# Performance work log

Measured on AMD Instinct MI355X. Metric: run time of the kernel, lower is better.

## Reference

```python
import jax, jax.numpy as jnp
import numpy as np

EPS = 1e-5
RES = [12000, 9000, 6000, 4000]
CH = [9, 64, 128, 256]
SKIPS = 3
FC_N = 128


def batchnorm(x, g, b):
    # train-mode BatchNorm2d over (batch, face) dims; x: [B, C, F]
    m = x.mean(axis=(0, 2), keepdims=True)
    v = x.var(axis=(0, 2), keepdims=True)
    xn = (x - m) * jax.lax.rsqrt(v + EPS)
    return xn * g[None, :, None] + b[None, :, None]


def mesh_conv(x, nbr, w):
    # x: [B, C, F]; nbr: [F, 3] neighbor face ids; w: [O, C, 4]
    n = x[:, :, nbr]                      # [B, C, F, 3] irregular gather
    n1, n2, n3 = n[..., 0], n[..., 1], n[..., 2]
    G = jnp.stack([
        x,
        n1 + n2 + n3,
        jnp.abs(n1 - n2) + jnp.abs(n2 - n3) + jnp.abs(n3 - n1),
        jnp.maximum(jnp.maximum(n1, n2), n3),
    ], axis=-1)                           # [B, C, F, 4] symmetric features
    return jnp.einsum('ocj,bcfj->bof', w, G)


def mres_conv(x, nbr, wc, ws, bng, bnb):
    # MResConvFace: conv0 -> skips x (bn(relu) -> conv) -> +skip -> relu
    x = mesh_conv(x, nbr, wc)
    x1 = x
    for i in range(SKIPS):
        x = batchnorm(jax.nn.relu(x), bng[i], bnb[i])
        x = mesh_conv(x, nbr, ws[i])
    return jax.nn.relu(x + x1)


def setup_inputs() -> dict:
    key = jax.random.key(0)
    ks = jax.random.split(key, 64)
    it = iter(range(64))
    d = {}
    d['x'] = jax.random.normal(ks[next(it)], (8, CH[0], RES[0]), dtype=jnp.float32)
    for i in range(3):
        d[f'nbr{i}'] = jax.random.randint(ks[next(it)], (RES[i], 3), 0, RES[i], dtype=jnp.int32)
        d[f'pool{i}'] = jax.random.randint(ks[next(it)], (RES[i + 1], 3), 0, RES[i], dtype=jnp.int32)
    for i in range(3):
        cin, cout = CH[i], CH[i + 1]
        d[f'wc{i}'] = jax.random.normal(ks[next(it)], (cout, cin, 4), dtype=jnp.float32) * (1.0 / np.sqrt(4 * cin))
        d[f'ws{i}'] = jax.random.normal(ks[next(it)], (SKIPS, cout, cout, 4), dtype=jnp.float32) * (1.0 / np.sqrt(4 * cout))
        d[f'bng{i}'] = jnp.ones((SKIPS, cout), dtype=jnp.float32)
        d[f'bnb{i}'] = jnp.zeros((SKIPS, cout), dtype=jnp.float32)
        d[f'ng{i}'] = jnp.ones((cout,), dtype=jnp.float32)
        d[f'nb{i}'] = jnp.zeros((cout,), dtype=jnp.float32)
    d['fc1_w'] = jax.random.normal(ks[next(it)], (FC_N, CH[-1]), dtype=jnp.float32) * (1.0 / np.sqrt(CH[-1]))
    d['fc1_b'] = jnp.zeros((FC_N,), dtype=jnp.float32)
    d['fc2_w'] = jax.random.normal(ks[next(it)], (1, FC_N), dtype=jnp.float32) * (1.0 / np.sqrt(FC_N))
    d['fc2_b'] = jnp.zeros((1,), dtype=jnp.float32)
    return d


def reference(x, nbr0, nbr1, nbr2, pool0, pool1, pool2,
              wc0, ws0, bng0, bnb0, ng0, nb0,
              wc1, ws1, bng1, bnb1, ng1, nb1,
              wc2, ws2, bng2, bnb2, ng2, nb2,
              fc1_w, fc1_b, fc2_w, fc2_b):
    nbrs = [nbr0, nbr1, nbr2]
    pools = [pool0, pool1, pool2]
    wcs, wss = [wc0, wc1, wc2], [ws0, ws1, ws2]
    bngs, bnbs = [bng0, bng1, bng2], [bnb0, bnb1, bnb2]
    ngs, nbs = [ng0, ng1, ng2], [nb0, nb1, nb2]
    for i in range(3):
        x = mres_conv(x, nbrs[i], wcs[i], wss[i], bngs[i], bnbs[i])
        x = jax.nn.relu(batchnorm(x, ngs[i], nbs[i]))
        x = x[:, :, pools[i]].mean(axis=-1)   # MeshPoolFace: collapse 3 faces -> 1
    x = x.mean(axis=-1)                        # global AvgPool1d over faces -> [B, C]
    h = jax.nn.relu(x @ fc1_w.T + fc1_b)
    return jax.nn.sigmoid(h @ fc2_w.T + fc2_b)  # [B, 1]
```

## Files before the change

kernel.cpp:

```cpp
#include <hip/hip_runtime.h>
#include <math.h>

#define NPART 64
#define TILE_F 16

typedef unsigned short u16;
typedef __attribute__((ext_vector_type(8))) short short8;
typedef __attribute__((ext_vector_type(4))) float f32x4;

__device__ __forceinline__ float relu_(float v){ return fmaxf(v, 0.f); }

__device__ __forceinline__ u16 f2bf(float x){
  unsigned u = __float_as_uint(x);
  u = (u + 0x7fffu + ((u >> 16) & 1u)) >> 16;
  return (u16)u;
}

static __device__ __forceinline__ f32x4 mfma_bf16(short8 a, short8 b, f32x4 c){
  asm("v_mfma_f32_16x16x32_bf16 %0, %1, %2, %0" : "+v"(c) : "v"(a), "v"(b));
  return c;
}

template<int CIN,int COUT,int WR,int NWR,bool BN,bool STATS,bool RES>
__global__ __launch_bounds__(NWR*(COUT/64)*64) void mconv_kernel(
    const float* __restrict__ xin, const int* __restrict__ nbr,
    const u16* __restrict__ wbf,
    const float* __restrict__ ps_in, const float* __restrict__ gamma,
    const float* __restrict__ beta, const float* __restrict__ res,
    float* __restrict__ out, float* __restrict__ psum,
    int F, float invN)
{
  constexpr int nWc = COUT/64;
  constexpr int T   = NWR*nWc*64;
  constexpr int BR  = NWR*WR;
  constexpr int K   = 4*CIN;
  constexpr int NSTEP = CIN/16;
  constexpr int ITEMS = (BR*4)/T;
  constexpr int NRF   = WR/16;

  __shared__ __align__(16) u16 Gs[2][BR*64];
  __shared__ float ls[STATS?COUT:1], lq[STATS?COUT:1];
  __shared__ float aS[BN?CIN:1], dS[BN?CIN:1];

  const int t=threadIdx.x, lane=t&63, wid=t>>6;
  const int wm=wid/nWc, wc=wid%nWc;
  const int l15=lane&15, kq=lane>>4;

  const int batch = blockIdx.x & 7;
  const int row0  = (blockIdx.x >> 3) * BR;

  if (BN){
    for (int c=t;c<CIN;c+=T){
      float s=0.f,q=0.f;
      #pragma unroll 4
      for (int p=0;p<NPART;p++){ s+=ps_in[p*256+c]; q+=ps_in[(NPART+p)*256+c]; }
      float m=s*invN, v=q*invN-m*m;
      float ai=gamma[c]*rsqrtf(v+1e-5f);
      aS[c]=ai; dS[c]=beta[c]-m*ai;
    }
  }
  if (STATS){ for (int i=t;i<COUT;i+=T){ ls[i]=0.f; lq[i]=0.f; } }
  __syncthreads();

  const float *P0[ITEMS],*P1[ITEMS],*P2[ITEMS],*P3[ITEMS];
  #pragma unroll
  for (int i=0;i<ITEMS;i++){
    int idx=i*T+t, gr=idx>>2, c4q=idx&3;
    int f=row0+gr;
    if (f>=F) f=F-1;
    int i1=nbr[f*3+0], i2=nbr[f*3+1], i3=nbr[f*3+2];
    const float* xb=xin+(size_t)batch*F*CIN+c4q*4;
    P0[i]=xb+(size_t)f *CIN; P1[i]=xb+(size_t)i1*CIN;
    P2[i]=xb+(size_t)i2*CIN; P3[i]=xb+(size_t)i3*CIN;
  }

  const u16* wp = wbf + (size_t)(wc*64+l15)*K + kq*8;
  auto BLD=[&](int cg,int j)->short8{
    return *(const short8*)(wp + (size_t)cg*16*K + (size_t)j*32);
  };
  auto ADS=[&](int pb,int rr,int h)->short8{
    int r=wm*WR+rr*16+l15;
    int sl=h*4+kq;
    return *(const short8*)&Gs[pb][(size_t)r*64 + (size_t)((sl^(r&7))*8)];
  };
  auto GLD=[&](int s,float4 (&g)[ITEMS][4]){
    #pragma unroll
    for (int i=0;i<ITEMS;i++){
      g[i][0]=*(const float4*)(P0[i]+s*16);
      g[i][1]=*(const float4*)(P1[i]+s*16);
      g[i][2]=*(const float4*)(P2[i]+s*16);
      g[i][3]=*(const float4*)(P3[i]+s*16);
    }
  };
  auto BLDW=[&](int pb,int s,float4 (&g)[ITEMS][4]){
    #pragma unroll
    for (int i=0;i<ITEMS;i++){
      int idx=i*T+t, gr=idx>>2, c4q=idx&3;
      float4 S=g[i][0],N1=g[i][1],N2=g[i][2],N3=g[i][3];
      if (BN){
        float4 a4=*(const float4*)&aS[s*16+c4q*4];
        float4 d4=*(const float4*)&dS[s*16+c4q*4];
        S.x =fmaf(relu_(S.x ),a4.x,d4.x); S.y =fmaf(relu_(S.y ),a4.y,d4.y);
        S.z =fmaf(relu_(S.z ),a4.z,d4.z); S.w =fmaf(relu_(S.w ),a4.w,d4.w);
        N1.x=fmaf(relu_(N1.x),a4.x,d4.x); N1.y=fmaf(relu_(N1.y),a4.y,d4.y);
        N1.z=fmaf(relu_(N1.z),a4.z,d4.z); N1.w=fmaf(relu_(N1.w),a4.w,d4.w);
        N2.x=fmaf(relu_(N2.x),a4.x,d4.x); N2.y=fmaf(relu_(N2.y),a4.y,d4.y);
        N2.z=fmaf(relu_(N2.z),a4.z,d4.z); N2.w=fmaf(relu_(N2.w),a4.w,d4.w);
        N3.x=fmaf(relu_(N3.x),a4.x,d4.x); N3.y=fmaf(relu_(N3.y),a4.y,d4.y);
        N3.z=fmaf(relu_(N3.z),a4.z,d4.z); N3.w=fmaf(relu_(N3.w),a4.w,d4.w);
      }
      short8 lo,hi;
      #define FEAT(dst,i0,sv,av,bv,cv) \
        dst[i0+0]=(short)f2bf(sv); \
        dst[i0+1]=(short)f2bf(av+bv+cv); \
        dst[i0+2]=(short)f2bf(fabsf(av-bv)+fabsf(bv-cv)+fabsf(cv-av)); \
        dst[i0+3]=(short)f2bf(fmaxf(fmaxf(av,bv),cv));
      FEAT(lo,0,S.x,N1.x,N2.x,N3.x)
      FEAT(lo,4,S.y,N1.y,N2.y,N3.y)
      FEAT(hi,0,S.z,N1.z,N2.z,N3.z)
      FEAT(hi,4,S.w,N1.w,N2.w,N3.w)
      #undef FEAT
      u16* rowp=&Gs[pb][(size_t)gr*64];
      *(short8*)&rowp[(size_t)(((2*c4q  )^(gr&7))*8)]=lo;
      *(short8*)&rowp[(size_t)(((2*c4q+1)^(gr&7))*8)]=hi;
    }
  };

  f32x4 acc[NRF][4];
  #pragma unroll
  for (int rr=0;rr<NRF;rr++)
    #pragma unroll
    for (int cg=0;cg<4;cg++){ f32x4 z={0.f,0.f,0.f,0.f}; acc[rr][cg]=z; }

  short8 B0[4],B1[4];
  #pragma unroll
  for (int cg=0;cg<4;cg++) B0[cg]=BLD(cg,0);
  #pragma unroll
  for (int cg=0;cg<4;cg++) B1[cg]=BLD(cg,1);

  { float4 g0[ITEMS][4]; GLD(0,g0); BLDW(0,0,g0); }
  __syncthreads();

  #pragma unroll 2
  for (int s=0;s<NSTEP;s++){
    const int pb=s&1;
    float4 g[ITEMS][4];
    if (s+1<NSTEP) GLD(s+1,g);
    short8 A[NRF];
    #pragma unroll
    for (int rr=0;rr<NRF;rr++) A[rr]=ADS(pb,rr,0);
    #pragma unroll
    for (int rr=0;rr<NRF;rr++)
      #pragma unroll
      for (int cg=0;cg<4;cg++) acc[rr][cg]=mfma_bf16(A[rr],B0[cg],acc[rr][cg]);
    if (s+1<NSTEP){
      #pragma unroll
      for (int cg=0;cg<4;cg++) B0[cg]=BLD(cg,2*(s+1));
    }
    #pragma unroll
    for (int rr=0;rr<NRF;rr++) A[rr]=ADS(pb,rr,1);
    #pragma unroll
    for (int rr=0;rr<NRF;rr++)
      #pragma unroll
      for (int cg=0;cg<4;cg++) acc[rr][cg]=mfma_bf16(A[rr],B1[cg],acc[rr][cg]);
    if (s+1<NSTEP){
      #pragma unroll
      for (int cg=0;cg<4;cg++) B1[cg]=BLD(cg,2*(s+1)+1);
      BLDW(pb^1,s+1,g);
    }
    __syncthreads();
  }

  const size_t bbase=(size_t)batch*F;
  #pragma unroll
  for (int cg=0;cg<4;cg++){
    const int col=wc*64+cg*16+l15;
    float rs=0.f,rq=0.f;
    #pragma unroll
    for (int rr=0;rr<NRF;rr++){
      const int r0=row0 + wm*WR + rr*16 + kq*4;
      #pragma unroll
      for (int q=0;q<4;q++){
        int r=r0+q;
        if (r<F){
          size_t idx=(bbase+r)*COUT+col;
          float v=acc[rr][cg][q];
          if (RES){ v += res[idx]; v = relu_(v); }
          out[idx]=v;
          if (STATS){ float rv = RES ? v : relu_(v); rs+=rv; rq+=rv*rv; }
        }
      }
    }
    if (STATS){ atomicAdd(&ls[col],rs); atomicAdd(&lq[col],rq); }
  }
  if (STATS){
    __syncthreads();
    const int part=blockIdx.x&(NPART-1);
    for (int i=t;i<COUT;i+=T){
      atomicAdd(&psum[(size_t)part*256+i],ls[i]);
      atomicAdd(&psum[(size_t)(NPART+part)*256+i],lq[i]);
    }
  }
}

template<int CIN,int COUT,bool BN,bool STATS>
__global__ __launch_bounds__(256) void conv_kernel(
    const float* __restrict__ xin, const int* __restrict__ nbr,
    const float* __restrict__ Wt, const float* __restrict__ bn_a,
    const float* __restrict__ bn_d,
    float* __restrict__ out, float* __restrict__ psum, int F)
{
  constexpr int K = 4*CIN;
  constexpr int ROWLEN = K + 4;
  __shared__ float Gs[TILE_F][ROWLEN];
  __shared__ int   nI[TILE_F*3];
  __shared__ float ls[STATS?COUT:1];
  __shared__ float lq[STATS?COUT:1];
  const int t = threadIdx.x;
  const int fbase = blockIdx.x*TILE_F;
  const int b = blockIdx.y;
  const float* __restrict__ xb = xin + (size_t)b*F*CIN;

  if (t < TILE_F*3){ int fi=t/3, j=t-fi*3; int fg=fbase+fi; nI[t]=(fg<F)?nbr[fg*3+j]:0; }
  if (STATS){ for (int i=t;i<COUT;i+=256){ ls[i]=0.f; lq[i]=0.f; } }
  __syncthreads();

  for (int idx=t; idx<TILE_F*CIN; idx+=256){
    int fi=idx/CIN, c=idx-fi*CIN;
    int fg=fbase+fi;
    float* dst=&Gs[fi][4*c];
    if (fg<F){
      int i1=nI[fi*3], i2=nI[fi*3+1], i3=nI[fi*3+2];
      float s =xb[(size_t)fg*CIN+c];
      float v1=xb[(size_t)i1*CIN+c];
      float v2=xb[(size_t)i2*CIN+c];
      float v3=xb[(size_t)i3*CIN+c];
      if (BN){ float a=bn_a[c], dd=bn_d[c];
        s=fmaf(relu_(s),a,dd); v1=fmaf(relu_(v1),a,dd);
        v2=fmaf(relu_(v2),a,dd); v3=fmaf(relu_(v3),a,dd); }
      dst[0]=s; dst[1]=v1+v2+v3;
      dst[2]=fabsf(v1-v2)+fabsf(v2-v3)+fabsf(v3-v1);
      dst[3]=fmaxf(fmaxf(v1,v2),v3);
    } else { dst[0]=0.f;dst[1]=0.f;dst[2]=0.f;dst[3]=0.f; }
  }
  __syncthreads();

  constexpr int OQ=COUT/4;
  constexpr int R=256/OQ;
  constexpr int FPT=TILE_F/R;
  const int col=t%OQ, row=t/OQ;
  const int o0=col*4, f0=row*FPT;
  float4 acc[FPT];
  #pragma unroll
  for (int fi=0;fi<FPT;fi++){ acc[fi].x=0.f;acc[fi].y=0.f;acc[fi].z=0.f;acc[fi].w=0.f; }

  for (int k=0;k<K;k+=4){
    float4 w0=*(const float4*)&Wt[(size_t)(k+0)*COUT+o0];
    float4 w1=*(const float4*)&Wt[(size_t)(k+1)*COUT+o0];
    float4 w2=*(const float4*)&Wt[(size_t)(k+2)*COUT+o0];
    float4 w3=*(const float4*)&Wt[(size_t)(k+3)*COUT+o0];
    #pragma unroll
    for (int fi=0;fi<FPT;fi++){
      float4 g=*(const float4*)&Gs[f0+fi][k];
      acc[fi].x=fmaf(g.x,w0.x,fmaf(g.y,w1.x,fmaf(g.z,w2.x,fmaf(g.w,w3.x,acc[fi].x))));
      acc[fi].y=fmaf(g.x,w0.y,fmaf(g.y,w1.y,fmaf(g.z,w2.y,fmaf(g.w,w3.y,acc[fi].y))));
      acc[fi].z=fmaf(g.x,w0.z,fmaf(g.y,w1.z,fmaf(g.z,w2.z,fmaf(g.w,w3.z,acc[fi].z))));
      acc[fi].w=fmaf(g.x,w0.w,fmaf(g.y,w1.w,fmaf(g.z,w2.w,fmaf(g.w,w3.w,acc[fi].w))));
    }
  }

  float4 rs={0,0,0,0}, rq={0,0,0,0};
  #pragma unroll
  for (int fi=0;fi<FPT;fi++){
    int fg=fbase+f0+fi;
    if (fg<F){
      *(float4*)&out[((size_t)b*F+fg)*COUT+o0]=acc[fi];
      if (STATS){
        float rx=relu_(acc[fi].x), ry=relu_(acc[fi].y);
        float rz=relu_(acc[fi].z), rw=relu_(acc[fi].w);
        rs.x+=rx; rs.y+=ry; rs.z+=rz; rs.w+=rw;
        rq.x+=rx*rx; rq.y+=ry*ry; rq.z+=rz*rz; rq.w+=rw*rw;
      }
    }
  }
  if (STATS){
    atomicAdd(&ls[o0+0],rs.x); atomicAdd(&ls[o0+1],rs.y);
    atomicAdd(&ls[o0+2],rs.z); atomicAdd(&ls[o0+3],rs.w);
    atomicAdd(&lq[o0+0],rq.x); atomicAdd(&lq[o0+1],rq.y);
    atomicAdd(&lq[o0+2],rq.z); atomicAdd(&lq[o0+3],rq.w);
    __syncthreads();
    int part=(blockIdx.y*gridDim.x+blockIdx.x)&(NPART-1);
    for (int i=t;i<COUT;i+=256){
      atomicAdd(&psum[(size_t)part*256+i], ls[i]);
      atomicAdd(&psum[(size_t)(NPART+part)*256+i], lq[i]);
    }
  }
}

__global__ __launch_bounds__(256) void pool_kernel(
    const float* __restrict__ z, const int* __restrict__ pl,
    const float* __restrict__ ps_in, const float* __restrict__ gamma,
    const float* __restrict__ beta,
    float* __restrict__ out, int C4, int F, int Fn, int n4, float invN)
{
  __shared__ float aS[256], dS[256];
  const int C=C4*4;
  const int t=threadIdx.x;
  if (t<C){
    float s=0.f,q=0.f;
    #pragma unroll 4
    for (int p=0;p<NPART;p++){ s+=ps_in[p*256+t]; q+=ps_in[(NPART+p)*256+t]; }
    float m=s*invN, v=q*invN-m*m;
    float ai=gamma[t]*rsqrtf(v+1e-5f);
    aS[t]=ai; dS[t]=beta[t]-m*ai;
  }
  __syncthreads();
  for (int i=blockIdx.x*256+t; i<n4; i+=gridDim.x*256){
    int c4=i%C4; int rest=i/C4; int p=rest%Fn; int b=rest/Fn;
    int p0=pl[p*3], p1=pl[p*3+1], p2=pl[p*3+2];
    float4 a4=*(const float4*)&aS[4*c4], d4=*(const float4*)&dS[4*c4];
    float4 v0=*(const float4*)&z[((size_t)b*F+p0)*C+4*c4];
    float4 v1=*(const float4*)&z[((size_t)b*F+p1)*C+4*c4];
    float4 v2=*(const float4*)&z[((size_t)b*F+p2)*C+4*c4];
    float4 r;
    r.x=(relu_(fmaf(v0.x,a4.x,d4.x))+relu_(fmaf(v1.x,a4.x,d4.x))+relu_(fmaf(v2.x,a4.x,d4.x)))*(1.f/3.f);
    r.y=(relu_(fmaf(v0.y,a4.y,d4.y))+relu_(fmaf(v1.y,a4.y,d4.y))+relu_(fmaf(v2.y,a4.y,d4.y)))*(1.f/3.f);
    r.z=(relu_(fmaf(v0.z,a4.z,d4.z))+relu_(fmaf(v1.z,a4.z,d4.z))+relu_(fmaf(v2.z,a4.z,d4.z)))*(1.f/3.f);
    r.w=(relu_(fmaf(v0.w,a4.w,d4.w))+relu_(fmaf(v1.w,a4.w,d4.w))+relu_(fmaf(v2.w,a4.w,d4.w)))*(1.f/3.f);
    *(float4*)&out[((size_t)b*Fn+p)*C+4*c4]=r;
  }
}

__global__ __launch_bounds__(256) void colsum_kernel(
    const float* __restrict__ x, float* __restrict__ bc, int F, int chunk)
{
  int b=blockIdx.y; int f0=blockIdx.x*chunk;
  int c=threadIdx.x;
  int fe=f0+chunk; if (fe>F) fe=F;
  float s=0.f;
  for (int f=f0;f<fe;f++) s+=x[((size_t)b*F+f)*256+c];
  atomicAdd(&bc[b*256+c], s);
}

__global__ __launch_bounds__(256) void head_kernel(
    const float* __restrict__ bc, const float* __restrict__ w1,
    const float* __restrict__ b1, const float* __restrict__ w2,
    const float* __restrict__ b2, float* __restrict__ outp, float invF)
{
  __shared__ float xm[8*256];
  __shared__ float h[8*128];
  int t=threadIdx.x;
  for (int i=t;i<2048;i+=256) xm[i]=bc[i]*invF;
  __syncthreads();
  #pragma unroll
  for (int r=0;r<4;r++){
    int idx=t+r*256; int b=idx>>7, j=idx&127;
    float s=b1[j];
    for (int c=0;c<256;c++) s=fmaf(xm[b*256+c],w1[j*256+c],s);
    h[idx]=relu_(s);
  }
  __syncthreads();
  if (t<8){
    float s=b2[0];
    for (int j=0;j<128;j++) s=fmaf(h[t*128+j],w2[j],s);
    outp[t]=1.f/(1.f+expf(-s));
  }
}

__global__ __launch_bounds__(256) void transpose_in_kernel(
    const float* __restrict__ x, float* __restrict__ xt, int F)
{
  int i=blockIdx.x*256+threadIdx.x;
  int total=8*9*F;
  if (i<total){ int f=i%F; int c=(i/F)%9; int b=i/(9*F);
    xt[((size_t)b*F+f)*9+c]=x[i]; }
}

__global__ __launch_bounds__(256) void transpose_w_kernel(
    const float* __restrict__ w, float* __restrict__ wt, int K, int COUT)
{
  int i=blockIdx.x*256+threadIdx.x;
  if (i<K*COUT){ int o=i/K, k=i-o*K; wt[(size_t)k*COUT+o]=w[i]; }
}

__global__ __launch_bounds__(256) void cvt_bf16_kernel(
    const float* __restrict__ w, u16* __restrict__ o, int n)
{
  int i=blockIdx.x*256+threadIdx.x;
  if (i<n) o[i]=f2bf(w[i]);
}


template<int CIN,int COUT,int WR,int NWR,bool BN,bool STATS,bool RES>
static void launch_mconv(const float* xin, const int* nbr, const u16* wbf,
                         const float* ps_in, const float* gamma, const float* beta,
                         const float* res, float* out, float* ps_out,
                         int F, float invN, hipStream_t stream)
{
  constexpr int T  = NWR*(COUT/64)*64;
  constexpr int BR = NWR*WR;
  int nb = (F + BR - 1)/BR;
  mconv_kernel<CIN,COUT,WR,NWR,BN,STATS,RES><<<8*nb, T, 0, stream>>>(
      xin,nbr,wbf,ps_in,gamma,beta,res,out,ps_out,F,invN);
}

extern "C" void kernel_launch(void* const* d_in, const int* in_sizes, int n_in,
                              void* d_out, int out_size, void* d_ws, size_t ws_size,
                              hipStream_t stream)
{
  const float* x    =(const float*)d_in[0];
  const int*  nbr0  =(const int*)d_in[1];
  const int*  pool0 =(const int*)d_in[2];
  const int*  nbr1  =(const int*)d_in[3];
  const int*  pool1 =(const int*)d_in[4];
  const int*  nbr2  =(const int*)d_in[5];
  const int*  pool2 =(const int*)d_in[6];
  const float* wc0  =(const float*)d_in[7];
  const float* ws0  =(const float*)d_in[8];
  const float* bng0 =(const float*)d_in[9];
  const float* bnb0 =(const float*)d_in[10];
  const float* ng0  =(const float*)d_in[11];
  const float* nb0  =(const float*)d_in[12];
  const float* wc1  =(const float*)d_in[13];
  const float* ws1  =(const float*)d_in[14];
  const float* bng1 =(const float*)d_in[15];
  const float* bnb1 =(const float*)d_in[16];
  const float* ng1  =(const float*)d_in[17];
  const float* nb1  =(const float*)d_in[18];
  const float* wc2  =(const float*)d_in[19];
  const float* ws2  =(const float*)d_in[20];
  const float* bng2 =(const float*)d_in[21];
  const float* bnb2 =(const float*)d_in[22];
  const float* ng2  =(const float*)d_in[23];
  const float* nb2  =(const float*)d_in[24];
  const float* fc1w =(const float*)d_in[25];
  const float* fc1b =(const float*)d_in[26];
  const float* fc2w =(const float*)d_in[27];
  const float* fc2b =(const float*)d_in[28];
  float* outp=(float*)d_out;

  char* base=(char*)d_ws;
  size_t off=0;
  auto alloc=[&](size_t nbytes)->void*{
    void* p=base+off; off=(off+nbytes+255)&~(size_t)255; return p; };

  float* psum0 =(float*)alloc((size_t)12*131072);
  float* bc    =(float*)alloc(8192);
  float* wt_wc0=(float*)alloc((size_t)36*64*4);
  u16*   bws0  =(u16*)alloc((size_t)3*16384*2);
  u16*   bwc1  =(u16*)alloc((size_t)32768*2);
  u16*   bws1  =(u16*)alloc((size_t)3*65536*2);
  u16*   bwc2  =(u16*)alloc((size_t)131072*2);
  u16*   bws2  =(u16*)alloc((size_t)3*262144*2);
  float* xT    =(float*)alloc((size_t)8*12000*9*4);
  float* B0    =(float*)alloc((size_t)49152000);
  float* B1    =(float*)alloc((size_t)49152000);
  float* B2    =(float*)alloc((size_t)49152000);
  if (off>ws_size) return;

  auto PS=[&](int i){ return psum0+(size_t)i*32768; };

  hipMemsetAsync(psum0,0,(size_t)12*131072+8192,stream);

  { int n=8*9*12000; transpose_in_kernel<<<(n+255)/256,256,0,stream>>>(x,xT,12000); }
  { int n=36*64; transpose_w_kernel<<<(n+255)/256,256,0,stream>>>(wc0,wt_wc0,36,64); }
  auto cv=[&](const float* w,u16* o,int n){
    cvt_bf16_kernel<<<(n+255)/256,256,0,stream>>>(w,o,n); };
  cv(ws0,bws0,3*16384);
  cv(wc1,bwc1,32768);
  cv(ws1,bws1,3*65536);
  cv(wc2,bwc2,131072);
  cv(ws2,bws2,3*262144);

  {
    const int F=12000; const float invN=1.f/(8.f*F);
    dim3 grid((F+TILE_F-1)/TILE_F, 8);
    conv_kernel<9,64,false,true><<<grid,256,0,stream>>>(xT,nbr0,wt_wc0,nullptr,nullptr,B0,PS(0),F);
    launch_mconv<64,64,32,2,true,true ,false>(B0,nbr0,bws0,        PS(0),bng0,     bnb0,     nullptr,B1,PS(1),F,invN,stream);
    launch_mconv<64,64,32,2,true,true ,false>(B1,nbr0,bws0+16384,  PS(1),bng0+64,  bnb0+64,  nullptr,B2,PS(2),F,invN,stream);
    launch_mconv<64,64,32,2,true,true ,true >(B2,nbr0,bws0+32768,  PS(2),bng0+128, bnb0+128, B0,     B1,PS(3),F,invN,stream);
    int n4p=8*9000*16; int gp=(n4p+255)/256; if (gp>2048) gp=2048;
    pool_kernel<<<gp,256,0,stream>>>(B1,pool0,PS(3),ng0,nb0,B2,16,F,9000,n4p,invN);
  }
  {
    const int F=9000; const float invN=1.f/(8.f*F);
    launch_mconv<64,128,64,1,false,true ,false>(B2,nbr1,bwc1,         nullptr,nullptr,  nullptr,  nullptr,B0,PS(4),F,invN,stream);
    launch_mconv<128,128,64,1,true,true ,false>(B0,nbr1,bws1,         PS(4),bng1,      bnb1,     nullptr,B1,PS(5),F,invN,stream);
    launch_mconv<128,128,64,1,true,true ,false>(B1,nbr1,bws1+65536,   PS(5),bng1+128,  bnb1+128, nullptr,B2,PS(6),F,invN,stream);
    launch_mconv<128,128,64,1,true,true ,true >(B2,nbr1,bws1+131072,  PS(6),bng1+256,  bnb1+256, B0,     B1,PS(7),F,invN,stream);
    int n4p=8*6000*32; int gp=(n4p+255)/256; if (gp>2048) gp=2048;
    pool_kernel<<<gp,256,0,stream>>>(B1,pool1,PS(7),ng1,nb1,B0,32,F,6000,n4p,invN);
  }
  {
    const int F=6000; const float invN=1.f/(8.f*F);
    launch_mconv<128,256,64,1,false,true ,false>(B0,nbr2,bwc2,         nullptr,nullptr,  nullptr,  nullptr,B1,PS(8),F,invN,stream);
    launch_mconv<256,256,64,1,true,true ,false>(B1,nbr2,bws2,         PS(8), bng2,     bnb2,     nullptr,B2,PS(9),F,invN,stream);
    launch_mconv<256,256,64,1,true,true ,false>(B2,nbr2,bws2+262144,  PS(9), bng2+256, bnb2+256, nullptr,B0,PS(10),F,invN,stream);
    launch_mconv<256,256,64,1,true,true ,true >(B0,nbr2,bws2+524288,  PS(10),bng2+512, bnb2+512, B1,     B2,PS(11),F,invN,stream);
    int n4p=8*4000*64; int gp=(n4p+255)/256; if (gp>2048) gp=2048;
    pool_kernel<<<gp,256,0,stream>>>(B2,pool2,PS(11),ng2,nb2,B0,64,F,4000,n4p,invN);
    colsum_kernel<<<dim3(16,8),256,0,stream>>>(B0,bc,4000,250);
  }
  head_kernel<<<1,256,0,stream>>>(bc,fc1w,fc1b,fc2w,fc2b,outp,1.f/4000.f);
}
```

Baseline: 918.4 us.

## Split output channels across blocks in mesh conv kernels

Adds a CSPLIT template parameter so each block computes only a slice of the output channels, and the grid grows by that factor. Stages 2 and 3 now split output channels in two, and stage 2 also moves to 2 warp-rows of 32 faces. This raises block count and occupancy and lowers per-block register and thread count. In exchange, each channel block rebuilds the same gathered neighbor features, so the gather work and loads of the input activations are duplicated.

```diff
diff --git a/kernel.cpp b/kernel.cpp
--- a/kernel.cpp
+++ b/kernel.cpp
@@ -21,8 +21,8 @@
   return c;
 }
 
-template<int CIN,int COUT,int WR,int NWR,bool BN,bool STATS,bool RES>
-__global__ __launch_bounds__(NWR*(COUT/64)*64) void mconv_kernel(
+template<int CIN,int COUT,int CSPLIT,int WR,int NWR,bool BN,bool STATS,bool RES>
+__global__ __launch_bounds__(NWR*(COUT/CSPLIT/64)*64) void mconv_kernel(
     const float* __restrict__ xin, const int* __restrict__ nbr,
     const u16* __restrict__ wbf,
     const float* __restrict__ ps_in, const float* __restrict__ gamma,
@@ -30,7 +30,8 @@
     float* __restrict__ out, float* __restrict__ psum,
     int F, float invN)
 {
-  constexpr int nWc = COUT/64;
+  constexpr int CW  = COUT/CSPLIT;
+  constexpr int nWc = CW/64;
   constexpr int T   = NWR*nWc*64;
   constexpr int BR  = NWR*WR;
   constexpr int K   = 4*CIN;
@@ -39,7 +40,7 @@
   constexpr int NRF   = WR/16;
 
   __shared__ __align__(16) u16 Gs[2][BR*64];
-  __shared__ float ls[STATS?COUT:1], lq[STATS?COUT:1];
+  __shared__ float ls[STATS?CW:1], lq[STATS?CW:1];
   __shared__ float aS[BN?CIN:1], dS[BN?CIN:1];
 
   const int t=threadIdx.x, lane=t&63, wid=t>>6;
@@ -47,7 +48,10 @@
   const int l15=lane&15, kq=lane>>4;
 
   const int batch = blockIdx.x & 7;
-  const int row0  = (blockIdx.x >> 3) * BR;
+  const int rest  = blockIdx.x >> 3;
+  const int cblk  = rest % CSPLIT;
+  const int row0  = (rest / CSPLIT) * BR;
+  const int col0  = cblk*CW;
 
   if (BN){
     for (int c=t;c<CIN;c+=T){
@@ -59,7 +63,7 @@
       aS[c]=ai; dS[c]=beta[c]-m*ai;
     }
   }
-  if (STATS){ for (int i=t;i<COUT;i+=T){ ls[i]=0.f; lq[i]=0.f; } }
+  if (STATS){ for (int i=t;i<CW;i+=T){ ls[i]=0.f; lq[i]=0.f; } }
   __syncthreads();
 
   const float *P0[ITEMS],*P1[ITEMS],*P2[ITEMS],*P3[ITEMS];
@@ -74,7 +78,7 @@
     P2[i]=xb+(size_t)i2*CIN; P3[i]=xb+(size_t)i3*CIN;
   }
 
-  const u16* wp = wbf + (size_t)(wc*64+l15)*K + kq*8;
+  const u16* wp = wbf + (size_t)(col0 + wc*64 + l15)*K + kq*8;
   auto BLD=[&](int cg,int j)->short8{
     return *(const short8*)(wp + (size_t)cg*16*K + (size_t)j*32);
   };
@@ -174,7 +178,8 @@
   const size_t bbase=(size_t)batch*F;
   #pragma unroll
   for (int cg=0;cg<4;cg++){
-    const int col=wc*64+cg*16+l15;
+    const int cl=wc*64+cg*16+l15;
+    const int col=col0+cl;
     float rs=0.f,rq=0.f;
     #pragma unroll
     for (int rr=0;rr<NRF;rr++){
@@ -191,14 +196,14 @@
         }
       }
     }
-    if (STATS){ atomicAdd(&ls[col],rs); atomicAdd(&lq[col],rq); }
+    if (STATS){ atomicAdd(&ls[cl],rs); atomicAdd(&lq[cl],rq); }
   }
   if (STATS){
     __syncthreads();
     const int part=blockIdx.x&(NPART-1);
-    for (int i=t;i<COUT;i+=T){
-      atomicAdd(&psum[(size_t)part*256+i],ls[i]);
-      atomicAdd(&psum[(size_t)(NPART+part)*256+i],lq[i]);
+    for (int i=t;i<CW;i+=T){
+      atomicAdd(&psum[(size_t)part*256+col0+i],ls[i]);
+      atomicAdd(&psum[(size_t)(NPART+part)*256+col0+i],lq[i]);
     }
   }
 }
@@ -391,16 +396,16 @@
 }
 
 
-template<int CIN,int COUT,int WR,int NWR,bool BN,bool STATS,bool RES>
+template<int CIN,int COUT,int CSPLIT,int WR,int NWR,bool BN,bool STATS,bool RES>
 static void launch_mconv(const float* xin, const int* nbr, const u16* wbf,
                          const float* ps_in, const float* gamma, const float* beta,
                          const float* res, float* out, float* ps_out,
                          int F, float invN, hipStream_t stream)
 {
-  constexpr int T  = NWR*(COUT/64)*64;
+  constexpr int T  = NWR*(COUT/CSPLIT/64)*64;
   constexpr int BR = NWR*WR;
   int nb = (F + BR - 1)/BR;
-  mconv_kernel<CIN,COUT,WR,NWR,BN,STATS,RES><<<8*nb, T, 0, stream>>>(
+  mconv_kernel<CIN,COUT,CSPLIT,WR,NWR,BN,STATS,RES><<<8*nb*CSPLIT, T, 0, stream>>>(
       xin,nbr,wbf,ps_in,gamma,beta,res,out,ps_out,F,invN);
 }
 
@@ -476,27 +481,27 @@
     const int F=12000; const float invN=1.f/(8.f*F);
     dim3 grid((F+TILE_F-1)/TILE_F, 8);
     conv_kernel<9,64,false,true><<<grid,256,0,stream>>>(xT,nbr0,wt_wc0,nullptr,nullptr,B0,PS(0),F);
-    launch_mconv<64,64,32,2,true,true ,false>(B0,nbr0,bws0,        PS(0),bng0,     bnb0,     nullptr,B1,PS(1),F,invN,stream);
-    launch_mconv<64,64,32,2,true,true ,false>(B1,nbr0,bws0+16384,  PS(1),bng0+64,  bnb0+64,  nullptr,B2,PS(2),F,invN,stream);
-    launch_mconv<64,64,32,2,true,true ,true >(B2,nbr0,bws0+32768,  PS(2),bng0+128, bnb0+128, B0,     B1,PS(3),F,invN,stream);
+    launch_mconv<64,64,1,32,2,true,true ,false>(B0,nbr0,bws0,        PS(0),bng0,     bnb0,     nullptr,B1,PS(1),F,invN,stream);
+    launch_mconv<64,64,1,32,2,true,true ,false>(B1,nbr0,bws0+16384,  PS(1),bng0+64,  bnb0+64,  nullptr,B2,PS(2),F,invN,stream);
+    launch_mconv<64,64,1,32,2,true,true ,true >(B2,nbr0,bws0+32768,  PS(2),bng0+128, bnb0+128, B0,     B1,PS(3),F,invN,stream);
     int n4p=8*9000*16; int gp=(n4p+255)/256; if (gp>2048) gp=2048;
     pool_kernel<<<gp,256,0,stream>>>(B1,pool0,PS(3),ng0,nb0,B2,16,F,9000,n4p,invN);
   }
   {
     const int F=9000; const float invN=1.f/(8.f*F);
-    launch_mconv<64,128,64,1,false,true ,false>(B2,nbr1,bwc1,         nullptr,nullptr,  nullptr,  nullptr,B0,PS(4),F,invN,stream);
-    launch_mconv<128,128,64,1,true,true ,false>(B0,nbr1,bws1,         PS(4),bng1,      bnb1,     nullptr,B1,PS(5),F,invN,stream);
-    launch_mconv<128,128,64,1,true,true ,false>(B1,nbr1,bws1+65536,   PS(5),bng1+128,  bnb1+128, nullptr,B2,PS(6),F,invN,stream);
-    launch_mconv<128,128,64,1,true,true ,true >(B2,nbr1,bws1+131072,  PS(6),bng1+256,  bnb1+256, B0,     B1,PS(7),F,invN,stream);
+    launch_mconv<64,128,2,32,2,false,true ,false>(B2,nbr1,bwc1,         nullptr,nullptr,  nullptr,  nullptr,B0,PS(4),F,invN,stream);
+    launch_mconv<128,128,2,32,2,true,true ,false>(B0,nbr1,bws1,         PS(4),bng1,      bnb1,     nullptr,B1,PS(5),F,invN,stream);
+    launch_mconv<128,128,2,32,2,true,true ,false>(B1,nbr1,bws1+65536,   PS(5),bng1+128,  bnb1+128, nullptr,B2,PS(6),F,invN,stream);
+    launch_mconv<128,128,2,32,2,true,true ,true >(B2,nbr1,bws1+131072,  PS(6),bng1+256,  bnb1+256, B0,     B1,PS(7),F,invN,stream);
     int n4p=8*6000*32; int gp=(n4p+255)/256; if (gp>2048) gp=2048;
     pool_kernel<<<gp,256,0,stream>>>(B1,pool1,PS(7),ng1,nb1,B0,32,F,6000,n4p,invN);
   }
   {
     const int F=6000; const float invN=1.f/(8.f*F);
-    launch_mconv<128,256,64,1,false,true ,false>(B0,nbr2,bwc2,         nullptr,nullptr,  nullptr,  nullptr,B1,PS(8),F,invN,stream);
-    launch_mconv<256,256,64,1,true,true ,false>(B1,nbr2,bws2,         PS(8), bng2,     bnb2,     nullptr,B2,PS(9),F,invN,stream);
-    launch_mconv<256,256,64,1,true,true ,false>(B2,nbr2,bws2+262144,  PS(9), bng2+256, bnb2+256, nullptr,B0,PS(10),F,invN,stream);
-    launch_mconv<256,256,64,1,true,true ,true >(B0,nbr2,bws2+524288,  PS(10),bng2+512, bnb2+512, B1,     B2,PS(11),F,invN,stream);
+    launch_mconv<128,256,2,64,1,false,true ,false>(B0,nbr2,bwc2,         nullptr,nullptr,  nullptr,  nullptr,B1,PS(8),F,invN,stream);
+    launch_mconv<256,256,2,64,1,true,true ,false>(B1,nbr2,bws2,         PS(8), bng2,     bnb2,     nullptr,B2,PS(9),F,invN,stream);
+    launch_mconv<256,256,2,64,1,true,true ,false>(B2,nbr2,bws2+262144,  PS(9), bng2+256, bnb2+256, nullptr,B0,PS(10),F,invN,stream);
+    launch_mconv<256,256,2,64,1,true,true ,true >(B0,nbr2,bws2+524288,  PS(10),bng2+512, bnb2+512, B1,     B2,PS(11),F,invN,stream);
     int n4p=8*4000*64; int gp=(n4p+255)/256; if (gp>2048) gp=2048;
     pool_kernel<<<gp,256,0,stream>>>(B2,pool2,PS(11),ng2,nb2,B0,64,F,4000,n4p,invN);
     colsum_kernel<<<dim3(16,8),256,0,stream>>>(B0,bc,4000,250);
```

After: 1.204 ms. 1.31x slower.
